# Optimization experiments

Measured on AMD Instinct MI355X. Metric: run time of the kernel, lower is better.

The kernel has to match this reference:

```python
import jax, jax.numpy as jnp
import numpy as np

N_NODES = 50000
N_EDGES = 800000
IN_CH = 128
HID = 128
N_GRAPHS = 512


def setup_inputs() -> dict:
    key = jax.random.key(0)
    ks = jax.random.split(key, 12)
    x = jax.random.normal(ks[0], (N_NODES, IN_CH), dtype=jnp.float32)
    edge_index = jax.random.randint(ks[1], (2, N_EDGES), 0, N_NODES, dtype=jnp.int64)
    batch = jnp.sort(jax.random.randint(ks[2], (N_NODES,), 0, N_GRAPHS, dtype=jnp.int64))
    s = 0.05
    params = {
        'W1l': jax.random.normal(ks[3], (HID, IN_CH), dtype=jnp.float32) * s,
        'W1r': jax.random.normal(ks[4], (HID, IN_CH), dtype=jnp.float32) * s,
        'b1': jax.random.normal(ks[5], (HID,), dtype=jnp.float32) * s,
        'W2l': jax.random.normal(ks[6], (HID, HID), dtype=jnp.float32) * s,
        'W2r': jax.random.normal(ks[7], (HID, HID), dtype=jnp.float32) * s,
        'b2': jax.random.normal(ks[8], (HID,), dtype=jnp.float32) * s,
        'W3l': jax.random.normal(ks[9], (HID, HID), dtype=jnp.float32) * s,
        'W3r': jax.random.normal(ks[10], (HID, HID), dtype=jnp.float32) * s,
        'b3': jax.random.normal(ks[11], (HID,), dtype=jnp.float32) * s,
    }
    return {'x': x, 'edge_index': edge_index, 'batch': batch, **params}


def reference(x, edge_index, batch, W1l, W1r, b1, W2l, W2r, b2, W3l, W3r, b3):
    src = edge_index[0]
    dst = edge_index[1]
    n = x.shape[0]
    # in-degree for mean aggregation (nodes with no in-edges get 0 aggregate)
    deg = jax.ops.segment_sum(jnp.ones((src.shape[0],), x.dtype), dst, num_segments=n)
    inv_deg = (1.0 / jnp.maximum(deg, 1.0))[:, None]  # [N,1]

    def sage(h, Wl, Wr, b):
        # gather neighbor feats, scatter-mean to targets, then linear + root term
        agg = jax.ops.segment_sum(h[src], dst, num_segments=n) * inv_deg  # [N,d]
        return agg @ Wl.T + h @ Wr.T + b

    h = jax.nn.relu(sage(x, W1l, W1r, b1))
    h = jax.nn.relu(sage(h, W2l, W2r, b2))
    h = jax.nn.relu(sage(h, W3l, W3r, b3))

    # global mean pool over graph ids
    counts = jax.ops.segment_sum(jnp.ones((n,), h.dtype), batch, num_segments=N_GRAPHS)
    pooled = jax.ops.segment_sum(h, batch, num_segments=N_GRAPHS)
    return pooled / jnp.maximum(counts, 1.0)[:, None]
```

## Files before the change

### kernel.cpp

```cpp
#include <hip/hip_runtime.h>

#define N_NODES 50000
#define NP 50048
#define N_EDGES 800000
#define N_GRAPHS 512
#define F 128
#define ELLW 64

#define FILL_BLOCKS 3125
#define CASTX_BLOCKS 3128
#define CASTW_BLOCKS 48

typedef __bf16 bf16x8 __attribute__((ext_vector_type(8)));
typedef float f32x4 __attribute__((ext_vector_type(4)));
typedef unsigned short ushort_t;
typedef unsigned int uint_t;

__device__ inline ushort_t f2bf(float f) {
    uint_t u = __float_as_uint(f);
    u += 0x7FFFu + ((u >> 16) & 1u);
    return (ushort_t)(u >> 16);
}
__device__ inline float bf2f(ushort_t u) {
    return __uint_as_float(((uint_t)u) << 16);
}
__device__ inline uint_t pack2(float a, float b) {
    return (uint_t)f2bf(a) | ((uint_t)f2bf(b) << 16);
}
__device__ inline void addrow(float* a, uint4 v) {
    a[0] += __uint_as_float(v.x << 16); a[1] += __uint_as_float(v.x & 0xFFFF0000u);
    a[2] += __uint_as_float(v.y << 16); a[3] += __uint_as_float(v.y & 0xFFFF0000u);
    a[4] += __uint_as_float(v.z << 16); a[5] += __uint_as_float(v.z & 0xFFFF0000u);
    a[6] += __uint_as_float(v.w << 16); a[7] += __uint_as_float(v.w & 0xFFFF0000u);
}

__global__ __launch_bounds__(256) void k_build(
    const float* __restrict__ x,
    const float* __restrict__ w0, const float* __restrict__ w1,
    const float* __restrict__ w2, const float* __restrict__ w3,
    const float* __restrict__ w4, const float* __restrict__ w5,
    const int* __restrict__ src, const int* __restrict__ dst,
    ushort_t* __restrict__ X, ushort_t* __restrict__ WB,
    int* __restrict__ cnt, ushort_t* __restrict__ ell) {
    int b = blockIdx.x;
    int t = threadIdx.x;
    if (b < FILL_BLOCKS) {
        int e = b * 256 + t;
        int d = dst[e];
        int pos = atomicAdd(&cnt[d], 1);
        if (pos < ELLW) ell[((size_t)d << 6) + pos] = (ushort_t)src[e];
    } else if (b < FILL_BLOCKS + CASTX_BLOCKS) {
        int i = ((b - FILL_BLOCKS) * 256 + t) * 8;
        uint4 o = make_uint4(0, 0, 0, 0);
        if (i < N_NODES * F) {
            float4 v0 = *(const float4*)&x[i];
            float4 v1 = *(const float4*)&x[i + 4];
            o = make_uint4(pack2(v0.x, v0.y), pack2(v0.z, v0.w),
                           pack2(v1.x, v1.y), pack2(v1.z, v1.w));
        }
        *(uint4*)&X[i] = o;
    } else {
        int idx = (b - FILL_BLOCKS - CASTX_BLOCKS) * 256 + t;
        int m = idx >> 11;
        int o = (idx & 2047) * 8;
        const float* s = w0;
        if (m == 1) s = w1; else if (m == 2) s = w2; else if (m == 3) s = w3;
        else if (m == 4) s = w4; else if (m == 5) s = w5;
        float4 v0 = *(const float4*)&s[o];
        float4 v1 = *(const float4*)&s[o + 4];
        *(uint4*)&WB[m * 16384 + o] =
            make_uint4(pack2(v0.x, v0.y), pack2(v0.z, v0.w),
                       pack2(v1.x, v1.y), pack2(v1.z, v1.w));
    }
}

__global__ __launch_bounds__(256) void k_gather(const ushort_t* __restrict__ h,
                                                const ushort_t* __restrict__ ell,
                                                const int* __restrict__ cnt,
                                                ushort_t* __restrict__ agg) {
    int t = blockIdx.x * 256 + threadIdx.x;
    int n = t >> 4;
    int lane16 = t & 15;
    if (n >= N_NODES) return;
    int deg = min(cnt[n], ELLW);
    const ushort_t* el = ell + ((size_t)n << 6);
    const uint4* h4 = (const uint4*)h;
    float ax[8], ay[8];
#pragma unroll
    for (int j = 0; j < 8; j++) { ax[j] = 0.f; ay[j] = 0.f; }
    int i = 0;
    for (; i + 4 <= deg; i += 4) {
        int s0 = el[i], s1 = el[i + 1], s2 = el[i + 2], s3 = el[i + 3];
        uint4 v0 = h4[(size_t)s0 * 16 + lane16];
        uint4 v1 = h4[(size_t)s1 * 16 + lane16];
        uint4 v2 = h4[(size_t)s2 * 16 + lane16];
        uint4 v3 = h4[(size_t)s3 * 16 + lane16];
        addrow(ax, v0); addrow(ay, v1); addrow(ax, v2); addrow(ay, v3);
    }
    for (; i < deg; i++) {
        uint4 v0 = h4[(size_t)el[i] * 16 + lane16];
        addrow(ax, v0);
    }
    float sc = 1.0f / fmaxf((float)deg, 1.0f);
    ((uint4*)agg)[(size_t)n * 16 + lane16] = make_uint4(
        pack2((ax[0] + ay[0]) * sc, (ax[1] + ay[1]) * sc),
        pack2((ax[2] + ay[2]) * sc, (ax[3] + ay[3]) * sc),
        pack2((ax[4] + ay[4]) * sc, (ax[5] + ay[5]) * sc),
        pack2((ax[6] + ay[6]) * sc, (ax[7] + ay[7]) * sc));
}

__global__ __launch_bounds__(256) void k_linear(const ushort_t* __restrict__ agg,
                                                const ushort_t* h,
                                                const ushort_t* __restrict__ Wl,
                                                const ushort_t* __restrict__ Wr,
                                                const float* __restrict__ bias,
                                                ushort_t* out) {
    __shared__ uint4 Alds4[1024];
    __shared__ uint4 Blds4[2048];
    ushort_t* Alds = (ushort_t*)Alds4;
    ushort_t* Blds = (ushort_t*)Blds4;

    int t = threadIdx.x;
    int w = t >> 6;
    int lane = t & 63;
    int bm = blockIdx.x * 64;
    int wm = (w & 1) * 32;
    int wn = (w >> 1) * 64;
    int lrow = lane & 15;
    int kg = lane >> 4;

    f32x4 acc[2][4];
#pragma unroll
    for (int i = 0; i < 2; i++)
#pragma unroll
        for (int j = 0; j < 4; j++) acc[i][j] = (f32x4){0.f, 0.f, 0.f, 0.f};

#pragma unroll
    for (int iter = 0; iter < 2; iter++) {
        const ushort_t* A = iter ? h : agg;
        const ushort_t* W = iter ? Wr : Wl;

        __syncthreads();
#pragma unroll
        for (int p = 0; p < 4; p++) {
            int chunkA = p * 4 + w;
            const ushort_t* gA = A + (size_t)(bm + lane) * F + chunkA * 8;
            ushort_t* lA = Alds + (size_t)(chunkA * 64) * 8;
            __builtin_amdgcn_global_load_lds(
                (const __attribute__((address_space(1))) void*)gA,
                (__attribute__((address_space(3))) void*)lA, 16, 0, 0);
        }
#pragma unroll
        for (int p = 0; p < 8; p++) {
            int chunkB = p * 2 + (w >> 1);
            int rbase = (w & 1) * 64;
            const ushort_t* gB = W + (size_t)(rbase + lane) * F + chunkB * 8;
            ushort_t* lB = Blds + (size_t)(chunkB * 128 + rbase) * 8;
            __builtin_amdgcn_global_load_lds(
                (const __attribute__((address_space(1))) void*)gB,
                (__attribute__((address_space(3))) void*)lB, 16, 0, 0);
        }
        __syncthreads();

#pragma unroll
        for (int ks = 0; ks < 4; ks++) {
            bf16x8 af[2], bfr[4];
#pragma unroll
            for (int i = 0; i < 2; i++)
                af[i] = *(const bf16x8*)(Alds +
                    (size_t)((ks * 4 + kg) * 64 + wm + i * 16 + lrow) * 8);
#pragma unroll
            for (int j = 0; j < 4; j++)
                bfr[j] = *(const bf16x8*)(Blds +
                    (size_t)((ks * 4 + kg) * 128 + wn + j * 16 + lrow) * 8);
#pragma unroll
            for (int i = 0; i < 2; i++)
#pragma unroll
                for (int j = 0; j < 4; j++)
                    acc[i][j] = __builtin_amdgcn_mfma_f32_16x16x32_bf16(
                        af[i], bfr[j], acc[i][j], 0, 0, 0);
        }
    }

    int quad = lane >> 4;
#pragma unroll
    for (int j = 0; j < 4; j++) {
        int c = wn + j * 16 + lrow;
        float bj = bias[c];
#pragma unroll
        for (int i = 0; i < 2; i++) {
#pragma unroll
            for (int r = 0; r < 4; r++) {
                int row = bm + wm + i * 16 + quad * 4 + r;
                if (row < N_NODES) {
                    float v = fmaxf(acc[i][j][r] + bj, 0.0f);
                    out[(size_t)row * F + c] = f2bf(v);
                }
            }
        }
    }
}

__global__ __launch_bounds__(256) void k_pool(const ushort_t* __restrict__ h,
                                              const int* __restrict__ batch,
                                              float* __restrict__ out) {
    __shared__ float red[128];
    int g = blockIdx.x;
    int t = threadIdx.x;
    int col = t & 127;
    int half = t >> 7;
    int lo = 0, hi = N_NODES;
    while (lo < hi) {
        int m = (lo + hi) >> 1;
        if (batch[m] < g) lo = m + 1; else hi = m;
    }
    int start = lo;
    lo = start; hi = N_NODES;
    while (lo < hi) {
        int m = (lo + hi) >> 1;
        if (batch[m] < g + 1) lo = m + 1; else hi = m;
    }
    int end = lo;
    float s = 0.0f;
    for (int n = start + half; n < end; n += 2)
        s += bf2f(h[(size_t)n * F + col]);
    if (half) red[col] = s;
    __syncthreads();
    if (!half)
        out[g * F + col] = (s + red[col]) / fmaxf((float)(end - start), 1.0f);
}

extern "C" void kernel_launch(void* const* d_in, const int* in_sizes, int n_in,
                              void* d_out, int out_size, void* d_ws, size_t ws_size,
                              hipStream_t stream) {
    const float* x   = (const float*)d_in[0];
    const int*   ei  = (const int*)d_in[1];
    const int* batch = (const int*)d_in[2];
    const float* W1l = (const float*)d_in[3];
    const float* W1r = (const float*)d_in[4];
    const float* b1  = (const float*)d_in[5];
    const float* W2l = (const float*)d_in[6];
    const float* W2r = (const float*)d_in[7];
    const float* b2  = (const float*)d_in[8];
    const float* W3l = (const float*)d_in[9];
    const float* W3r = (const float*)d_in[10];
    const float* b3  = (const float*)d_in[11];
    float* out = (float*)d_out;

    const int* src = ei;
    const int* dst = ei + N_EDGES;

    ushort_t* X   = (ushort_t*)d_ws;
    ushort_t* HA  = X + (size_t)NP * F;
    ushort_t* HB  = HA + (size_t)NP * F;
    ushort_t* AGG = HB + (size_t)NP * F;
    ushort_t* WB  = AGG + (size_t)NP * F;
    int* cnt = (int*)(WB + 6 * 16384);
    ushort_t* ell = (ushort_t*)(cnt + 50176);

    const ushort_t* Wb1l = WB;
    const ushort_t* Wb1r = WB + 16384;
    const ushort_t* Wb2l = WB + 2 * 16384;
    const ushort_t* Wb2r = WB + 3 * 16384;
    const ushort_t* Wb3l = WB + 4 * 16384;
    const ushort_t* Wb3r = WB + 5 * 16384;

    hipMemsetAsync(cnt, 0, 50176 * sizeof(int), stream);
    k_build<<<FILL_BLOCKS + CASTX_BLOCKS + CASTW_BLOCKS, 256, 0, stream>>>(
        x, W1l, W1r, W2l, W2r, W3l, W3r, src, dst, X, WB, cnt, ell);

    const int gatherBlocks = (N_NODES * 16 + 255) / 256;
    const int linearBlocks = NP / 64;

    k_gather<<<gatherBlocks, 256, 0, stream>>>(X, ell, cnt, AGG);
    k_linear<<<linearBlocks, 256, 0, stream>>>(AGG, X, Wb1l, Wb1r, b1, HA);
    k_gather<<<gatherBlocks, 256, 0, stream>>>(HA, ell, cnt, AGG);
    k_linear<<<linearBlocks, 256, 0, stream>>>(AGG, HA, Wb2l, Wb2r, b2, HB);
    k_gather<<<gatherBlocks, 256, 0, stream>>>(HB, ell, cnt, AGG);
    k_linear<<<linearBlocks, 256, 0, stream>>>(AGG, HB, Wb3l, Wb3r, b3, HA);

    k_pool<<<N_GRAPHS, 256, 0, stream>>>(HA, batch, out);
}
```

Baseline: 313.4 us.

## Fuse global mean pool into final linear kernel via LDS bins and last-block finalize

The separate pooling kernel is removed. The last SAGE linear layer now accumulates its ReLU outputs per graph into shared-memory bins, flushes them to a global pooled buffer with atomics, and lets the last-finishing block divide by the graph counts. This drops one launch and a re-read of the final hidden features. In exchange it adds float atomics, which make summation order nondeterministic, adds an extra memset region, and serialises the final division on a single block.

```diff
diff --git a/kernel.cpp b/kernel.cpp
--- a/kernel.cpp
+++ b/kernel.cpp
@@ -6,6 +6,8 @@
 #define N_GRAPHS 512
 #define F 128
 #define ELLW 64
+#define NTILES (NP / 64)
+#define SPAN 16
 
 #define FILL_BLOCKS 3125
 #define CASTX_BLOCKS 3128
@@ -109,12 +111,17 @@
         pack2((ax[6] + ay[6]) * sc, (ax[7] + ay[7]) * sc));
 }
 
+template <bool FUSE>
 __global__ __launch_bounds__(256) void k_linear(const ushort_t* __restrict__ agg,
                                                 const ushort_t* h,
                                                 const ushort_t* __restrict__ Wl,
                                                 const ushort_t* __restrict__ Wr,
                                                 const float* __restrict__ bias,
-                                                ushort_t* out) {
+                                                ushort_t* out,
+                                                const int* __restrict__ batch,
+                                                float* __restrict__ pooled,
+                                                int* __restrict__ doneCtr,
+                                                float* __restrict__ gout) {
     __shared__ uint4 Alds4[1024];
     __shared__ uint4 Blds4[2048];
     ushort_t* Alds = (ushort_t*)Alds4;
@@ -182,6 +189,15 @@
         }
     }
 
+    float* bins = (float*)Alds4;
+    int gmin = 0;
+    if constexpr (FUSE) {
+        __syncthreads();
+        for (int i = t; i < SPAN * F; i += 256) bins[i] = 0.f;
+        gmin = batch[bm];
+        __syncthreads();
+    }
+
     int quad = lane >> 4;
 #pragma unroll
     for (int j = 0; j < 4; j++) {
@@ -195,39 +211,54 @@
                 if (row < N_NODES) {
                     float v = fmaxf(acc[i][j][r] + bj, 0.0f);
                     out[(size_t)row * F + c] = f2bf(v);
+                    if constexpr (FUSE) {
+                        int b = batch[row] - gmin;
+                        if (b < SPAN) atomicAdd(&bins[b * F + c], v);
+                        else atomicAdd(&pooled[(size_t)(gmin + b) * F + c], v);
+                    }
                 }
             }
         }
     }
-}
-
-__global__ __launch_bounds__(256) void k_pool(const ushort_t* __restrict__ h,
-                                              const int* __restrict__ batch,
-                                              float* __restrict__ out) {
-    __shared__ float red[128];
-    int g = blockIdx.x;
-    int t = threadIdx.x;
-    int col = t & 127;
-    int half = t >> 7;
-    int lo = 0, hi = N_NODES;
-    while (lo < hi) {
-        int m = (lo + hi) >> 1;
-        if (batch[m] < g) lo = m + 1; else hi = m;
-    }
-    int start = lo;
-    lo = start; hi = N_NODES;
-    while (lo < hi) {
-        int m = (lo + hi) >> 1;
-        if (batch[m] < g + 1) lo = m + 1; else hi = m;
-    }
-    int end = lo;
-    float s = 0.0f;
-    for (int n = start + half; n < end; n += 2)
-        s += bf2f(h[(size_t)n * F + col]);
-    if (half) red[col] = s;
-    __syncthreads();
-    if (!half)
-        out[g * F + col] = (s + red[col]) / fmaxf((float)(end - start), 1.0f);
+
+    if constexpr (FUSE) {
+        __syncthreads();
+        int col = t & 127;
+        for (int b = t >> 7; b < SPAN; b += 2) {
+            float v = bins[b * F + col];
+            if (v != 0.f && gmin + b < N_GRAPHS)
+                atomicAdd(&pooled[(size_t)(gmin + b) * F + col], v);
+        }
+        __threadfence();
+        __syncthreads();
+        __shared__ int lastBlk;
+        if (t == 0) lastBlk = (atomicAdd(doneCtr, 1) == NTILES - 1) ? 1 : 0;
+        __syncthreads();
+        if (lastBlk) {
+            __threadfence();
+            float* cnts = (float*)Blds4;
+            for (int g = t; g < N_GRAPHS; g += 256) {
+                int lo = 0, hi = N_NODES;
+                while (lo < hi) {
+                    int m = (lo + hi) >> 1;
+                    if (batch[m] < g) lo = m + 1; else hi = m;
+                }
+                int start = lo;
+                lo = start; hi = N_NODES;
+                while (lo < hi) {
+                    int m = (lo + hi) >> 1;
+                    if (batch[m] < g + 1) lo = m + 1; else hi = m;
+                }
+                cnts[g] = fmaxf((float)(lo - start), 1.0f);
+            }
+            __syncthreads();
+            for (int i = t; i < N_GRAPHS * F; i += 256) {
+                float v = __hip_atomic_load(&pooled[i], __ATOMIC_RELAXED,
+                                            __HIP_MEMORY_SCOPE_AGENT);
+                gout[i] = v / cnts[i >> 7];
+            }
+        }
+    }
 }
 
 extern "C" void kernel_launch(void* const* d_in, const int* in_sizes, int n_in,
@@ -255,8 +286,10 @@
     ushort_t* HB  = HA + (size_t)NP * F;
     ushort_t* AGG = HB + (size_t)NP * F;
     ushort_t* WB  = AGG + (size_t)NP * F;
-    int* cnt = (int*)(WB + 6 * 16384);
-    ushort_t* ell = (ushort_t*)(cnt + 50176);
+    int* cnt      = (int*)(WB + 6 * 16384);
+    float* pooled = (float*)(cnt + 50176);
+    int* doneCtr  = (int*)(pooled + N_GRAPHS * F);
+    ushort_t* ell = (ushort_t*)(doneCtr + 16);
 
     const ushort_t* Wb1l = WB;
     const ushort_t* Wb1r = WB + 16384;
@@ -265,19 +298,20 @@
     const ushort_t* Wb3l = WB + 4 * 16384;
     const ushort_t* Wb3r = WB + 5 * 16384;
 
-    hipMemsetAsync(cnt, 0, 50176 * sizeof(int), stream);
+    hipMemsetAsync(cnt, 0, (50176 + N_GRAPHS * F + 16) * sizeof(int), stream);
     k_build<<<FILL_BLOCKS + CASTX_BLOCKS + CASTW_BLOCKS, 256, 0, stream>>>(
         x, W1l, W1r, W2l, W2r, W3l, W3r, src, dst, X, WB, cnt, ell);
 
     const int gatherBlocks = (N_NODES * 16 + 255) / 256;
-    const int linearBlocks = NP / 64;
+    const int linearBlocks = NTILES;
 
     k_gather<<<gatherBlocks, 256, 0, stream>>>(X, ell, cnt, AGG);
-    k_linear<<<linearBlocks, 256, 0, stream>>>(AGG, X, Wb1l, Wb1r, b1, HA);
+    k_linear<false><<<linearBlocks, 256, 0, stream>>>(
+        AGG, X, Wb1l, Wb1r, b1, HA, nullptr, nullptr, nullptr, nullptr);
     k_gather<<<gatherBlocks, 256, 0, stream>>>(HA, ell, cnt, AGG);
-    k_linear<<<linearBlocks, 256, 0, stream>>>(AGG, HA, Wb2l, Wb2r, b2, HB);
+    k_linear<false><<<linearBlocks, 256, 0, stream>>>(
+        AGG, HA, Wb2l, Wb2r, b2, HB, nullptr, nullptr, nullptr, nullptr);
     k_gather<<<gatherBlocks, 256, 0, stream>>>(HB, ell, cnt, AGG);
-    k_linear<<<linearBlocks, 256, 0, stream>>>(AGG, HB, Wb3l, Wb3r, b3, HA);
-
-    k_pool<<<N_GRAPHS, 256, 0, stream>>>(HA, batch, out);
-}
+    k_linear<true><<<linearBlocks, 256, 0, stream>>>(
+        AGG, HB, Wb3l, Wb3r, b3, HA, batch, pooled, doneCtr, out);
+}
```

New measurement: 465.2 us. 48.4% more time.
